# Kernel tuning notes

Hardware: AMD Instinct MI355X
Metric: run time of the kernel (lower is better)

## Reference

```python
import jax, jax.numpy as jnp
import numpy as np

N_NODES = 100000
N_EDGES = 1600000
C = 128          # in_channels
H = 32           # hidden MLP width
D = 1            # Dirichlet concentration dims
T = 3            # Taylor params (estimate_bpr=True)
JITTER = 1e-20


def gcn_conv(x, W, b, edge_index, n_nodes):
    """PyG GCNConv: add self-loops, symmetric normalization, aggregate to target."""
    h = x @ W                                   # [N, C] transform first (smaller than gathering raw x then transforming per-edge)
    src = jnp.concatenate([edge_index[0], jnp.arange(n_nodes)])
    dst = jnp.concatenate([edge_index[1], jnp.arange(n_nodes)])
    deg = jax.ops.segment_sum(jnp.ones_like(dst, dtype=h.dtype), dst, num_segments=n_nodes)
    dinv = jnp.where(deg > 0, jax.lax.rsqrt(deg), 0.0)
    norm = dinv[src] * dinv[dst]                # [E+N]
    msg = h[src] * norm[:, None]                # gather + scale  [E+N, C]
    out = jax.ops.segment_sum(msg, dst, num_segments=n_nodes)  # scatter-add
    return out + b


def setup_inputs() -> dict:
    key = jax.random.key(0)
    ks = jax.random.split(key, 20)
    s = 1.0 / np.sqrt(C)
    sh = 1.0 / np.sqrt(H)
    x = jax.random.normal(ks[0], (N_NODES, C), dtype=jnp.float32)
    edge_index = jax.random.randint(ks[1], (2, N_EDGES), 0, N_NODES)
    p = {
        "x": x, "edge_index": edge_index,
        # actor params
        "a_conv_W": jax.random.uniform(ks[2], (C, C), jnp.float32, -s, s),
        "a_conv_b": jnp.zeros((C,), jnp.float32),
        "a_l1_W": jax.random.uniform(ks[3], (C, H), jnp.float32, -s, s),
        "a_l1_b": jax.random.uniform(ks[4], (H,), jnp.float32, -s, s),
        "a_l2_W": jax.random.uniform(ks[5], (H, H), jnp.float32, -sh, sh),
        "a_l2_b": jax.random.uniform(ks[6], (H,), jnp.float32, -sh, sh),
        "a_l3_W": jax.random.uniform(ks[7], (H, D + T), jnp.float32, -sh, sh),
        "a_l3_b": jax.random.uniform(ks[8], (D + T,), jnp.float32, -sh, sh),
        # critic params
        "c_conv_W": jax.random.uniform(ks[9], (C, C), jnp.float32, -s, s),
        "c_conv_b": jnp.zeros((C,), jnp.float32),
        "c_l1_W": jax.random.uniform(ks[10], (C, H), jnp.float32, -s, s),
        "c_l1_b": jax.random.uniform(ks[11], (H,), jnp.float32, -s, s),
        "c_l2_W": jax.random.uniform(ks[12], (H, H), jnp.float32, -sh, sh),
        "c_l2_b": jax.random.uniform(ks[13], (H,), jnp.float32, -sh, sh),
        "c_l3_W": jax.random.uniform(ks[14], (H, 1), jnp.float32, -sh, sh),
        "c_l3_b": jax.random.uniform(ks[15], (1,), jnp.float32, -sh, sh),
    }
    return p


def reference(x, edge_index,
              a_conv_W, a_conv_b, a_l1_W, a_l1_b, a_l2_W, a_l2_b, a_l3_W, a_l3_b,
              c_conv_W, c_conv_b, c_l1_W, c_l1_b, c_l2_W, c_l2_b, c_l3_W, c_l3_b):
    n = x.shape[0]
    # ---- actor (GNNActor.forward) ----
    a = jax.nn.relu(gcn_conv(x, a_conv_W, a_conv_b, edge_index, n)) + x   # residual
    a = jax.nn.relu(a @ a_l1_W + a_l1_b)
    a = jax.nn.relu(a @ a_l2_W + a_l2_b)
    a_out = a @ a_l3_W + a_l3_b                      # [N, D+T]
    concentration = jax.nn.softplus(a_out[:, :D]).reshape(-1) + JITTER
    taylor_params = jax.nn.softplus(a_out[:, D:]) + JITTER
    # ---- critic (GNNCritic.forward) ----
    c = jax.nn.relu(gcn_conv(x, c_conv_W, c_conv_b, edge_index, n)) + x
    c = jnp.sum(c, axis=0)                           # graph readout [C]
    c = jax.nn.relu(c @ c_l1_W + c_l1_b)
    c = jax.nn.relu(c @ c_l2_W + c_l2_b)
    value = c @ c_l3_W + c_l3_b                      # [1]
    return concentration, taylor_params, value
```

## Files before the change

### kernel.cpp

```cpp
#include <hip/hip_runtime.h>
#include <math.h>

#define CCH 128
#define HID 32
#define SLOTS 64
#define NBINS 782
#define BSHIFT 7
#define BCAP 2432

typedef __attribute__((ext_vector_type(8))) short bf16x8;
typedef __attribute__((ext_vector_type(4))) float f32x4;

__device__ __forceinline__ unsigned bf16pk(float a, float b) {
    unsigned ua = __builtin_bit_cast(unsigned, a);
    unsigned ub = __builtin_bit_cast(unsigned, b);
    ua = (ua + 0x7FFFu + ((ua >> 16) & 1u)) >> 16;
    ub = (ub + 0x7FFFu + ((ub >> 16) & 1u)) >> 16;
    return ua | (ub << 16);
}
__device__ __forceinline__ unsigned short bf16s(float a) {
    unsigned ua = __builtin_bit_cast(unsigned, a);
    ua = (ua + 0x7FFFu + ((ua >> 16) & 1u)) >> 16;
    return (unsigned short)ua;
}
__device__ __forceinline__ float bflo(unsigned v) {
    return __builtin_bit_cast(float, v << 16);
}

__global__ void k_zero(const float* __restrict__ aW, const float* __restrict__ cW,
                       unsigned short* __restrict__ Wt,
                       float* __restrict__ csum, int* __restrict__ binCnt,
                       unsigned short* __restrict__ xsb, int N) {
    int t = threadIdx.x;
    if (blockIdx.x == 0) {
        if (t < CCH) csum[t] = 0.f;
        for (int i = t; i < NBINS; i += 256) binCnt[i] = 0;
        if (t < 64) ((unsigned*)xsb)[(long)N * 64 + t] = 0u;
        return;
    }
    int id = (blockIdx.x - 1) * 256 + t;
    int conv = id >> 14;
    int rem = id & 16383;
    int n = rem >> 7;
    int k = rem & 127;
    const float* W = conv ? cW : aW;
    Wt[id] = bf16s(W[k * CCH + n]);
}

__global__ __launch_bounds__(256, 4)
void k_bin(const int* __restrict__ ei, int E,
           int* __restrict__ binCnt, unsigned* __restrict__ stage) {
    int t = threadIdx.x;
    __shared__ int lcnt[NBINS];
    __shared__ int lofs[NBINS];
    const int nchunk = (E + 2047) / 2048;
    for (int ch = blockIdx.x; ch < nchunk; ch += gridDim.x) {
        int base = ch * 2048;
        for (int i = t; i < NBINS; i += 256) lcnt[i] = 0;
        __syncthreads();
        unsigned pk[8]; int bin[8];
#pragma unroll
        for (int k = 0; k < 8; k++) {
            int e = base + k * 256 + t;
            if (e < E) {
                unsigned src = (unsigned)ei[e];
                unsigned dst = (unsigned)ei[E + e];
                bin[k] = dst >> BSHIFT;
                pk[k] = src | ((dst & 0x7Fu) << 17);
                atomicAdd(&lcnt[bin[k]], 1);
            } else bin[k] = -1;
        }
        __syncthreads();
        for (int i = t; i < NBINS; i += 256) {
            int c = lcnt[i];
            lofs[i] = c ? atomicAdd(&binCnt[i], c) : 0;
        }
        __syncthreads();
#pragma unroll
        for (int k = 0; k < 8; k++) {
            if (bin[k] >= 0) {
                int pos = atomicAdd(&lofs[bin[k]], 1);
                if (pos < BCAP)
                    stage[(long)bin[k] * BCAP + pos] = pk[k];
            }
        }
        __syncthreads();
    }
}

__global__ __launch_bounds__(256)
void k_place(const unsigned* __restrict__ stage, const int* __restrict__ binCnt,
             const float* __restrict__ x, int* __restrict__ cnt,
             int* __restrict__ csr, unsigned short* __restrict__ xsb,
             float* __restrict__ csum, int N) {
    __shared__ int lcnt[128];
    __shared__ int lofs[128];
    __shared__ int lcur[128];
    __shared__ int wtot[2];
    __shared__ float scs[CCH];
    __shared__ unsigned ssrc[BCAP];
    __shared__ unsigned short sd8[BCAP];

    int t = threadIdx.x;
    int b = blockIdx.x;
    int count = binCnt[b];
    if (count > BCAP) count = BCAP;
    const unsigned* sp = stage + (long)b * BCAP;
    int dbase = b << BSHIFT;

    if (t < 128) lcnt[t] = 0;
    __syncthreads();
    for (int i = t; i < count; i += 256)
        atomicAdd(&lcnt[sp[i] >> 17], 1);
    __syncthreads();

    int craw = (t < 128) ? lcnt[t] : 0;
    int cc = craw > SLOTS ? SLOTS : craw;
    int lane = t & 63, wv = t >> 6;
    int xsc = cc;
#pragma unroll
    for (int d = 1; d < 64; d <<= 1) {
        int y = __shfl_up(xsc, d, 64);
        if (lane >= d) xsc += y;
    }
    if (t < 128 && lane == 63) wtot[wv] = xsc;
    __syncthreads();
    if (t < 128) {
        int pre = wv ? wtot[0] : 0;
        int excl = pre + xsc - cc;
        lofs[t] = excl;
        lcur[t] = excl;
        cnt[dbase + t] = craw;
    }
    __syncthreads();
    int total = wtot[0] + wtot[1];

    for (int i = t; i < count; i += 256) {
        unsigned p = sp[i];
        int d8 = (int)(p >> 17);
        int pos = atomicAdd(&lcur[d8], 1);
        if (pos - lofs[d8] < SLOTS) {
            ssrc[pos] = (p & 0x1FFFFu) << 5;
            sd8[pos] = (unsigned short)d8;
        }
    }
    __syncthreads();

    for (int i = t; i < total; i += 256) {
        int d8 = sd8[i];
        csr[(long)(dbase + d8) * SLOTS + (i - lofs[d8])] = (int)ssrc[i];
    }

    int rows = N - dbase; if (rows > 128) rows = 128;
    int nf4 = rows * 32;
    const float4* x4 = (const float4*)(x + (long)dbase * CCH);
    uint2* xo = (uint2*)xsb + (long)dbase * 32;
    float c0 = 0.f, c1 = 0.f, c2 = 0.f, c3 = 0.f;
    for (int i = t; i < nf4; i += 256) {
        float dv = rsqrtf((float)lcnt[i >> 5] + 1.0f);
        float4 v = x4[i];
        c0 += v.x; c1 += v.y; c2 += v.z; c3 += v.w;
        uint2 p;
        p.x = bf16pk(dv * v.x, dv * v.y);
        p.y = bf16pk(dv * v.z, dv * v.w);
        xo[i] = p;
    }
    if (t < CCH) scs[t] = 0.f;
    __syncthreads();
    int c4 = (t & 31) * 4;
    atomicAdd(&scs[c4 + 0], c0);
    atomicAdd(&scs[c4 + 1], c1);
    atomicAdd(&scs[c4 + 2], c2);
    atomicAdd(&scs[c4 + 3], c3);
    __syncthreads();
    if (t < CCH) atomicAdd(&csum[t], scs[t]);
}

__global__ __launch_bounds__(256, 4)
void k_gather_y(const unsigned short* __restrict__ xs,
                const int* __restrict__ cnt,
                const int* __restrict__ csr,
                unsigned short* __restrict__ yb, int N) {
    int t = threadIdx.x;
    int lane = t & 63;
    int wid = t >> 6;
    int half = lane >> 5;
    int hl = lane & 31;
    int wg = blockIdx.x * 4 + wid;
    int stride = gridDim.x * 4;
    const uint2* xu = (const uint2*)xs;
    uint2* yu = (uint2*)yb;
    int npairs = N >> 1;
    int zoff = N << 5;

    for (int p = wg; p < npairs; p += stride) {
        int nA = p * 2;
        int degr = cnt[nA + half];
        float dvd = rsqrtf((float)degr + 1.0f);
        int deg = degr > SLOTS ? SLOTS : degr;
        int degA = __builtin_amdgcn_readlane(deg, 0);
        int degB = __builtin_amdgcn_readlane(deg, 32);
        int dmax = degA > degB ? degA : degB;
        dmax = __builtin_amdgcn_readfirstlane(dmax);

        int idxl = csr[(long)nA * SLOTS + lane + (lane & 32)];
        if (hl >= deg) idxl = zoff;

        uint2 vs = xu[(long)nA * 32 + lane];
        float a0 = bflo(vs.x), a1 = __builtin_bit_cast(float, vs.x & 0xFFFF0000u);
        float a2 = bflo(vs.y), a3 = __builtin_bit_cast(float, vs.y & 0xFFFF0000u);

        int dm = dmax < 32 ? dmax : 32;
        int dm8 = (dm + 7) & ~7;
        for (int e = 0; e < dm8; e += 8) {
            uint2 v[8];
#pragma unroll
            for (int k = 0; k < 8; k++) {
                int iA = __builtin_amdgcn_readlane(idxl, e + k);
                int iB = __builtin_amdgcn_readlane(idxl, 32 + e + k);
                int boff = half ? iB : iA;
                v[k] = xu[boff + hl];
            }
#pragma unroll
            for (int k = 0; k < 8; k++) {
                a0 += bflo(v[k].x);
                a1 += __builtin_bit_cast(float, v[k].x);
                a2 += bflo(v[k].y);
                a3 += __builtin_bit_cast(float, v[k].y);
            }
        }
        if (dmax > 32) {
            int idxh = csr[(long)nA * SLOTS + lane + (lane & 32) + 32];
            if (hl + 32 >= deg) idxh = zoff;
            int dx8 = (dmax + 7) & ~7;
            for (int e = 32; e < dx8; e += 8) {
                uint2 w[8];
#pragma unroll
                for (int k = 0; k < 8; k++) {
                    int iA = __builtin_amdgcn_readlane(idxh, e - 32 + k);
                    int iB = __builtin_amdgcn_readlane(idxh, e + k);
                    int boff = half ? iB : iA;
                    w[k] = xu[boff + hl];
                }
#pragma unroll
                for (int k = 0; k < 8; k++) {
                    a0 += bflo(w[k].x);
                    a1 += __builtin_bit_cast(float, w[k].x);
                    a2 += bflo(w[k].y);
                    a3 += __builtin_bit_cast(float, w[k].y);
                }
            }
        }
        uint2 o;
        o.x = bf16pk(dvd * a0, dvd * a1);
        o.y = bf16pk(dvd * a2, dvd * a3);
        yu[(long)nA * 32 + lane] = o;
    }
}

__global__ __launch_bounds__(256, 4)
void k_gemm_y(const unsigned short* __restrict__ yb,
              const unsigned short* __restrict__ xs,
              const int* __restrict__ cnt,
              const unsigned short* __restrict__ Wt,
              const float* __restrict__ ab, const float* __restrict__ cb,
              unsigned short* __restrict__ a1b, float* __restrict__ csum,
              int N) {
    __shared__ unsigned short Ws[128 * 128];
    __shared__ float scs[CCH];
    int t = threadIdx.x;
    int row0 = blockIdx.x * 128;
    int wid = t >> 6, lane = t & 63;
    int m = lane & 15, quad = lane >> 4;
    int mrow0 = row0 + wid * 32;

    bf16x8 afr[2][4];
#pragma unroll
    for (int rt = 0; rt < 2; rt++) {
        int row = mrow0 + rt * 16 + m; if (row >= N) row = N - 1;
        const unsigned short* yr = yb + (long)row * CCH;
#pragma unroll
        for (int ks = 0; ks < 4; ks++)
            afr[rt][ks] = *(const bf16x8*)(yr + ks * 32 + quad * 8);
    }

    float rd0[4], rd1[4];
    {
        int r0 = mrow0 + quad * 4;
#pragma unroll
        for (int r = 0; r < 4; r++) {
            int ra = r0 + r;      if (ra >= N) ra = N - 1;
            int rb = r0 + 16 + r; if (rb >= N) rb = N - 1;
            rd0[r] = sqrtf((float)cnt[ra] + 1.0f);
            rd1[r] = sqrtf((float)cnt[rb] + 1.0f);
        }
    }

    for (int conv = 0; conv < 2; conv++) {
        __syncthreads();
        const uint4* src = (const uint4*)(Wt + conv * 16384);
#pragma unroll
        for (int i = 0; i < 8; i++) {
            int id = i * 256 + t;
            int n = id >> 4, c = id & 15;
            uint4 v = src[id];
            *(uint4*)(Ws + n * 128 + ((c ^ (n & 15)) * 8)) = v;
        }
        if (conv == 1 && t < CCH) scs[t] = 0.f;
        __syncthreads();

#pragma unroll
        for (int nt = 0; nt < 8; nt++) {
            int n = nt * 16 + m;
            f32x4 ac0 = {0.f, 0.f, 0.f, 0.f};
            f32x4 ac1 = {0.f, 0.f, 0.f, 0.f};
#pragma unroll
            for (int ks = 0; ks < 4; ks++) {
                bf16x8 b = *(const bf16x8*)(Ws + n * 128 + (((ks * 4 + quad) ^ m) * 8));
                ac0 = __builtin_amdgcn_mfma_f32_16x16x32_bf16(afr[0][ks], b, ac0, 0, 0, 0);
                ac1 = __builtin_amdgcn_mfma_f32_16x16x32_bf16(afr[1][ks], b, ac1, 0, 0, 0);
            }
            float bias = conv ? cb[n] : ab[n];
            float part = 0.f;
#pragma unroll
            for (int h = 0; h < 2; h++) {
#pragma unroll
                for (int r = 0; r < 4; r++) {
                    int row = mrow0 + quad * 4 + r + h * 16;
                    float acv = h ? ac1[r] : ac0[r];
                    if (row < N) {
                        if (conv == 0) {
                            float rd = h ? rd1[r] : rd0[r];
                            float xv = rd * bflo((unsigned)xs[(long)row * CCH + n]);
                            float v = fmaxf(acv + bias, 0.f) + xv;
                            a1b[(long)row * CCH + n] = bf16s(v);
                        } else {
                            part += fmaxf(acv + bias, 0.f);
                        }
                    }
                }
            }
            if (conv) atomicAdd(&scs[n], part);
        }
    }
    __syncthreads();
    if (t < CCH) atomicAdd(&csum[t], scs[t]);
}

__device__ __forceinline__ float softplus_f(float v) {
    return fmaxf(v, 0.f) + log1pf(expf(-fabsf(v)));
}

__global__ __launch_bounds__(256, 3)
void k_mlp(const unsigned short* __restrict__ a1b,
           const float* __restrict__ W1, const float* __restrict__ b1,
           const float* __restrict__ W2, const float* __restrict__ b2,
           const float* __restrict__ W3, const float* __restrict__ b3,
           const float* __restrict__ csum,
           const float* __restrict__ cW1, const float* __restrict__ cb1,
           const float* __restrict__ cW2, const float* __restrict__ cb2,
           const float* __restrict__ cW3, const float* __restrict__ cb3,
           float* __restrict__ out, int N) {
    __shared__ unsigned rowsW[64 * 65];
    __shared__ float h1L[64 * 33];
    __shared__ float h2L[64 * 33];
    int t = threadIdx.x;
    int l = t & 63;
    int w = t >> 6;
    long nbase = (long)blockIdx.x * 64;

    const uint4* ga = (const uint4*)(a1b + nbase * CCH);
#pragma unroll
    for (int i = 0; i < 4; i++) {
        int idx = i * 256 + t;
        int node = idx >> 4;
        int ch = idx & 15;
        uint4 v = make_uint4(0, 0, 0, 0);
        if (nbase + node < N) v = ga[node * 16 + ch];
        unsigned* dst = &rowsW[node * 65 + ch * 4];
        dst[0] = v.x; dst[1] = v.y; dst[2] = v.z; dst[3] = v.w;
    }
    __syncthreads();

    int j0 = __builtin_amdgcn_readfirstlane(w * 8);

    float h1[8];
#pragma unroll
    for (int j = 0; j < 8; j++) h1[j] = b1[j0 + j];
    for (int kp = 0; kp < 64; kp++) {
        unsigned v = rowsW[l * 65 + kp];
        float f0 = __builtin_bit_cast(float, v << 16);
        float f1 = __builtin_bit_cast(float, v & 0xFFFF0000u);
        const float* w0 = W1 + (2 * kp) * HID + j0;
        const float* w1 = W1 + (2 * kp + 1) * HID + j0;
#pragma unroll
        for (int j = 0; j < 8; j++)
            h1[j] = fmaf(f1, w1[j], fmaf(f0, w0[j], h1[j]));
    }
#pragma unroll
    for (int j = 0; j < 8; j++) h1L[l * 33 + j0 + j] = fmaxf(h1[j], 0.f);
    __syncthreads();

    float h2[8];
#pragma unroll
    for (int j = 0; j < 8; j++) h2[j] = b2[j0 + j];
    for (int k = 0; k < HID; k++) {
        float hv = h1L[l * 33 + k];
        const float* wr = W2 + k * HID + j0;
#pragma unroll
        for (int j = 0; j < 8; j++)
            h2[j] = fmaf(hv, wr[j], h2[j]);
    }
#pragma unroll
    for (int j = 0; j < 8; j++) h2L[l * 33 + j0 + j] = fmaxf(h2[j], 0.f);
    __syncthreads();

    if (w == 0) {
        long node = nbase + l;
        if (node < N) {
            float o[4] = {b3[0], b3[1], b3[2], b3[3]};
            for (int k = 0; k < HID; k++) {
                float hv = h2L[l * 33 + k];
#pragma unroll
                for (int m = 0; m < 4; m++)
                    o[m] = fmaf(hv, W3[k * 4 + m], o[m]);
            }
            out[node] = softplus_f(o[0]) + 1e-20f;
            float* ty = out + N;
            ty[node * 3 + 0] = softplus_f(o[1]) + 1e-20f;
            ty[node * 3 + 1] = softplus_f(o[2]) + 1e-20f;
            ty[node * 3 + 2] = softplus_f(o[3]) + 1e-20f;
        }
    }

    if (blockIdx.x == 0) {
        __syncthreads();
        float* cv  = h1L;
        float* hh1 = h2L;
        float* hh2 = h2L + 64;
        if (t < CCH) cv[t] = csum[t];
        __syncthreads();
        if (t < HID) {
            float a = cb1[t];
            for (int k = 0; k < CCH; k++) a = fmaf(cv[k], cW1[k * HID + t], a);
            hh1[t] = fmaxf(a, 0.f);
        }
        __syncthreads();
        if (t < HID) {
            float a = cb2[t];
            for (int k = 0; k < HID; k++) a = fmaf(hh1[k], cW2[k * HID + t], a);
            hh2[t] = fmaxf(a, 0.f);
        }
        __syncthreads();
        if (t == 0) {
            float a = cb3[0];
            for (int k = 0; k < HID; k++) a = fmaf(hh2[k], cW3[k], a);
            out[(long)4 * N] = a;
        }
    }
}

extern "C" void kernel_launch(void* const* d_in, const int* in_sizes, int n_in,
                              void* d_out, int out_size, void* d_ws, size_t ws_size,
                              hipStream_t stream) {
    const float* x   = (const float*)d_in[0];
    const int*   ei  = (const int*)d_in[1];
    const float* aW  = (const float*)d_in[2];
    const float* ab  = (const float*)d_in[3];
    const float* aW1 = (const float*)d_in[4];
    const float* ab1 = (const float*)d_in[5];
    const float* aW2 = (const float*)d_in[6];
    const float* ab2 = (const float*)d_in[7];
    const float* aW3 = (const float*)d_in[8];
    const float* ab3 = (const float*)d_in[9];
    const float* cW  = (const float*)d_in[10];
    const float* cb  = (const float*)d_in[11];
    const float* cW1 = (const float*)d_in[12];
    const float* cb1 = (const float*)d_in[13];
    const float* cW2 = (const float*)d_in[14];
    const float* cb2 = (const float*)d_in[15];
    const float* cW3 = (const float*)d_in[16];
    const float* cb3 = (const float*)d_in[17];
    float* out = (float*)d_out;

    const int N = in_sizes[0] / CCH;
    const int E = in_sizes[1] / 2;

    char* ws = (char*)d_ws;
    size_t off = 0;
    auto take = [&](size_t bytes) { void* p = ws + off; off += (bytes + 255) & ~(size_t)255; return p; };
    int*            cnt    = (int*)           take((size_t)NBINS * 128 * 4);
    int*            binCnt = (int*)           take(NBINS * 4);
    float*          csum   = (float*)         take(CCH * 4);
    unsigned short* Wt     = (unsigned short*)take(2 * 16384 * 2);
    int*            csr    = (int*)           take((size_t)N * SLOTS * 4);
    unsigned*       stage  = (unsigned*)      take((size_t)NBINS * BCAP * 4);
    unsigned short* xsb    = (unsigned short*)take((size_t)(N + 1) * CCH * 2);
    unsigned short* ybb    = (unsigned short*)take((size_t)N * CCH * 2);
    unsigned short* a1b    = (unsigned short*)take((size_t)N * CCH * 2);
    (void)ws_size;

    k_zero<<<129, 256, 0, stream>>>(aW, cW, Wt, csum, binCnt, xsb, N);
    k_bin<<<512, 256, 0, stream>>>(ei, E, binCnt, stage);
    k_place<<<NBINS, 256, 0, stream>>>(stage, binCnt, x, cnt, csr, xsb, csum, N);

    k_gather_y<<<2048, 256, 0, stream>>>(xsb, cnt, csr, ybb, N);

    const int gblocks = (N + 127) / 128;
    k_gemm_y<<<gblocks, 256, 0, stream>>>(ybb, xsb, cnt, Wt, ab, cb, a1b, csum, N);

    k_mlp<<<(N + 63) / 64, 256, 0, stream>>>(a1b, aW1, ab1, aW2, ab2, aW3, ab3,
                                             csum, cW1, cb1, cW2, cb2, cW3, cb3,
                                             out, N);
}
```

Measured before the change: 342.6 us.

## Split actor/critic GEMM across blocks and stage actor output through LDS for coalesced stores

The GEMM kernel now launches twice as many blocks, and each block handles either the actor or the critic convolution instead of looping over both. This removes the serialized second weight load and gives more parallelism. The actor path writes its ReLU outputs as bf16 into the shared weight buffer, then reads them back in row-major order. It then adds the degree-scaled residual and writes 16-byte vector stores instead of scattered 2-byte stores. The cost is that each block now loads the A fragments twice overall, and the actor path adds extra barriers inside its loop, including one per column tile.

```diff
diff --git a/kernel.cpp b/kernel.cpp
--- a/kernel.cpp
+++ b/kernel.cpp
@@ -25,6 +25,9 @@
 }
 __device__ __forceinline__ float bflo(unsigned v) {
     return __builtin_bit_cast(float, v << 16);
+}
+__device__ __forceinline__ float bfhiF(unsigned v) {
+    return __builtin_bit_cast(float, v & 0xFFFF0000u);
 }
 
 __global__ void k_zero(const float* __restrict__ aW, const float* __restrict__ cW,
@@ -207,8 +210,8 @@
         if (hl >= deg) idxl = zoff;
 
         uint2 vs = xu[(long)nA * 32 + lane];
-        float a0 = bflo(vs.x), a1 = __builtin_bit_cast(float, vs.x & 0xFFFF0000u);
-        float a2 = bflo(vs.y), a3 = __builtin_bit_cast(float, vs.y & 0xFFFF0000u);
+        float a0 = bflo(vs.x), a1 = bfhiF(vs.x);
+        float a2 = bflo(vs.y), a3 = bfhiF(vs.y);
 
         int dm = dmax < 32 ? dmax : 32;
         int dm8 = (dm + 7) & ~7;
@@ -265,11 +268,13 @@
               const unsigned short* __restrict__ Wt,
               const float* __restrict__ ab, const float* __restrict__ cb,
               unsigned short* __restrict__ a1b, float* __restrict__ csum,
-              int N) {
+              int N, int gblocks) {
     __shared__ unsigned short Ws[128 * 128];
     __shared__ float scs[CCH];
     int t = threadIdx.x;
-    int row0 = blockIdx.x * 128;
+    int bid = blockIdx.x;
+    int conv = bid >= gblocks ? 1 : 0;
+    int row0 = (conv ? bid - gblocks : bid) * 128;
     int wid = t >> 6, lane = t & 63;
     int m = lane & 15, quad = lane >> 4;
     int mrow0 = row0 + wid * 32;
@@ -284,20 +289,7 @@
             afr[rt][ks] = *(const bf16x8*)(yr + ks * 32 + quad * 8);
     }
 
-    float rd0[4], rd1[4];
     {
-        int r0 = mrow0 + quad * 4;
-#pragma unroll
-        for (int r = 0; r < 4; r++) {
-            int ra = r0 + r;      if (ra >= N) ra = N - 1;
-            int rb = r0 + 16 + r; if (rb >= N) rb = N - 1;
-            rd0[r] = sqrtf((float)cnt[ra] + 1.0f);
-            rd1[r] = sqrtf((float)cnt[rb] + 1.0f);
-        }
-    }
-
-    for (int conv = 0; conv < 2; conv++) {
-        __syncthreads();
         const uint4* src = (const uint4*)(Wt + conv * 16384);
 #pragma unroll
         for (int i = 0; i < 8; i++) {
@@ -306,9 +298,11 @@
             uint4 v = src[id];
             *(uint4*)(Ws + n * 128 + ((c ^ (n & 15)) * 8)) = v;
         }
-        if (conv == 1 && t < CCH) scs[t] = 0.f;
-        __syncthreads();
-
+        if (conv && t < CCH) scs[t] = 0.f;
+    }
+    __syncthreads();
+
+    if (conv == 0) {
 #pragma unroll
         for (int nt = 0; nt < 8; nt++) {
             int n = nt * 16 + m;
@@ -320,7 +314,58 @@
                 ac0 = __builtin_amdgcn_mfma_f32_16x16x32_bf16(afr[0][ks], b, ac0, 0, 0, 0);
                 ac1 = __builtin_amdgcn_mfma_f32_16x16x32_bf16(afr[1][ks], b, ac1, 0, 0, 0);
             }
-            float bias = conv ? cb[n] : ab[n];
+            float bias = ab[n];
+            __syncthreads();
+            unsigned short* reg = Ws + nt * 2048;
+#pragma unroll
+            for (int h = 0; h < 2; h++) {
+#pragma unroll
+                for (int r = 0; r < 4; r++) {
+                    int rl = wid * 32 + quad * 4 + r + h * 16;
+                    float acv = h ? ac1[r] : ac0[r];
+                    reg[rl * 16 + m] = bf16s(fmaxf(acv + bias, 0.f));
+                }
+            }
+        }
+        __syncthreads();
+#pragma unroll
+        for (int it = 0; it < 8; it++) {
+            int g = it * 256 + t;
+            int rl = g >> 4;
+            int c8 = g & 15;
+            int row = row0 + rl;
+            if (row < N) {
+                const unsigned short* lp = Ws + (c8 >> 1) * 2048 + rl * 16 + (c8 & 1) * 8;
+                uint4 lv = *(const uint4*)lp;
+                float rd = sqrtf((float)cnt[row] + 1.0f);
+                uint4 xv = *(const uint4*)(xs + (long)row * CCH + c8 * 8);
+                unsigned lw[4] = {lv.x, lv.y, lv.z, lv.w};
+                unsigned xw[4] = {xv.x, xv.y, xv.z, xv.w};
+                uint4 o;
+                unsigned ow[4];
+#pragma unroll
+                for (int q = 0; q < 4; q++) {
+                    float r0 = bflo(lw[q]) + rd * bflo(xw[q]);
+                    float r1 = bfhiF(lw[q]) + rd * bfhiF(xw[q]);
+                    ow[q] = bf16pk(r0, r1);
+                }
+                o.x = ow[0]; o.y = ow[1]; o.z = ow[2]; o.w = ow[3];
+                *(uint4*)(a1b + (long)row * CCH + c8 * 8) = o;
+            }
+        }
+    } else {
+#pragma unroll
+        for (int nt = 0; nt < 8; nt++) {
+            int n = nt * 16 + m;
+            f32x4 ac0 = {0.f, 0.f, 0.f, 0.f};
+            f32x4 ac1 = {0.f, 0.f, 0.f, 0.f};
+#pragma unroll
+            for (int ks = 0; ks < 4; ks++) {
+                bf16x8 b = *(const bf16x8*)(Ws + n * 128 + (((ks * 4 + quad) ^ m) * 8));
+                ac0 = __builtin_amdgcn_mfma_f32_16x16x32_bf16(afr[0][ks], b, ac0, 0, 0, 0);
+                ac1 = __builtin_amdgcn_mfma_f32_16x16x32_bf16(afr[1][ks], b, ac1, 0, 0, 0);
+            }
+            float bias = cb[n];
             float part = 0.f;
 #pragma unroll
             for (int h = 0; h < 2; h++) {
@@ -328,23 +373,14 @@
                 for (int r = 0; r < 4; r++) {
                     int row = mrow0 + quad * 4 + r + h * 16;
                     float acv = h ? ac1[r] : ac0[r];
-                    if (row < N) {
-                        if (conv == 0) {
-                            float rd = h ? rd1[r] : rd0[r];
-                            float xv = rd * bflo((unsigned)xs[(long)row * CCH + n]);
-                            float v = fmaxf(acv + bias, 0.f) + xv;
-                            a1b[(long)row * CCH + n] = bf16s(v);
-                        } else {
-                            part += fmaxf(acv + bias, 0.f);
-                        }
-                    }
+                    if (row < N) part += fmaxf(acv + bias, 0.f);
                 }
             }
-            if (conv) atomicAdd(&scs[n], part);
-        }
-    }
-    __syncthreads();
-    if (t < CCH) atomicAdd(&csum[t], scs[t]);
+            atomicAdd(&scs[n], part);
+        }
+        __syncthreads();
+        if (t < CCH) atomicAdd(&csum[t], scs[t]);
+    }
 }
 
 __device__ __forceinline__ float softplus_f(float v) {
@@ -507,7 +543,8 @@
     k_gather_y<<<2048, 256, 0, stream>>>(xsb, cnt, csr, ybb, N);
 
     const int gblocks = (N + 127) / 128;
-    k_gemm_y<<<gblocks, 256, 0, stream>>>(ybb, xsb, cnt, Wt, ab, cb, a1b, csum, N);
+    k_gemm_y<<<gblocks * 2, 256, 0, stream>>>(ybb, xsb, cnt, Wt, ab, cb, a1b,
+                                              csum, N, gblocks);
 
     k_mlp<<<(N + 63) / 64, 256, 0, stream>>>(a1b, aW1, ab1, aW2, ab2, aW3, ab3,
                                              csum, cW1, cb1, cW2, cb2, cW3, cb3,
```

Result: faster. 320.6 us (-6.4%).
